# Kernel tuning notes

Hardware: AMD Instinct MI355X
Metric: run time of the kernel (lower is better)

The kernel has to match this reference:

```python
import jax, jax.numpy as jnp
import numpy as np

NEG_SLOPE = 0.2
EPS = 1e-16


def gat_conv(x, edge_index, W, a_src, a_dst, b, heads, out_c, concat):
    # PyG GATConv: lin (no bias) -> per-head attention logits -> self-loops ->
    # leaky_relu -> softmax over incoming edges per dst -> weighted scatter-add -> bias
    N = x.shape[0]
    loop = jnp.arange(N)
    src = jnp.concatenate([edge_index[0], loop])  # [E+N]
    dst = jnp.concatenate([edge_index[1], loop])
    h = (x @ W).reshape(N, heads, out_c)                    # [N,H,C]
    a_s = jnp.sum(h * a_src[None], axis=-1)                 # [N,H]
    a_d = jnp.sum(h * a_dst[None], axis=-1)                 # [N,H]
    e = jax.nn.leaky_relu(a_s[src] + a_d[dst], NEG_SLOPE)   # [E+N,H]
    m = jax.ops.segment_max(e, dst, num_segments=N)         # stable softmax per dst
    e = jnp.exp(e - m[dst])
    s = jax.ops.segment_sum(e, dst, num_segments=N)
    alpha = e / (s[dst] + EPS)                              # [E+N,H]
    msg = h[src] * alpha[:, :, None]                        # [E+N,H,C]
    out = jax.ops.segment_sum(msg, dst, num_segments=N)     # [N,H,C]
    out = out.reshape(N, heads * out_c) if concat else out.mean(axis=1)
    return out + b


def setup_inputs() -> dict:
    key = jax.random.key(0)
    ks = jax.random.split(key, 20)
    N, E = 50000, 800000
    IN, HID, H, OUT = 128, 32, 4, 1
    HC = H * HID  # 128
    g = lambda k, shp: jax.random.normal(k, shp, dtype=jnp.float32) * 0.05
    inp = {
        "x": jax.random.normal(ks[0], (N, IN), dtype=jnp.float32),
        "edge_index": jax.random.randint(ks[1], (2, E), 0, N, dtype=jnp.int64),
        "batch": jnp.zeros((N,), dtype=jnp.int64),
        # conv0: GATConv(128 -> 32, heads=4, concat)
        "c0_w": g(ks[2], (IN, HC)), "c0_asrc": g(ks[3], (H, HID)),
        "c0_adst": g(ks[4], (H, HID)), "c0_b": jnp.zeros((HC,), jnp.float32),
        "s0_w": g(ks[5], (HC, IN)), "s0_b": jnp.zeros((HC,), jnp.float32),
        # conv1: GATConv(128 -> 32, heads=4, concat)
        "c1_w": g(ks[6], (HC, HC)), "c1_asrc": g(ks[7], (H, HID)),
        "c1_adst": g(ks[8], (H, HID)), "c1_b": jnp.zeros((HC,), jnp.float32),
        "s1_w": g(ks[9], (HC, HC)), "s1_b": jnp.zeros((HC,), jnp.float32),
        # conv2: GATConv(128 -> 1, heads=1, concat=False)
        "c2_w": g(ks[10], (HC, OUT)), "c2_asrc": g(ks[11], (1, OUT)),
        "c2_adst": g(ks[12], (1, OUT)), "c2_b": jnp.zeros((OUT,), jnp.float32),
        "s2_w": g(ks[13], (OUT, HC)), "s2_b": jnp.zeros((OUT,), jnp.float32),
    }
    return inp


def reference(x, edge_index, batch,
              c0_w, c0_asrc, c0_adst, c0_b, s0_w, s0_b,
              c1_w, c1_asrc, c1_adst, c1_b, s1_w, s1_b,
              c2_w, c2_asrc, c2_adst, c2_b, s2_w, s2_b):
    # layer 0 (dropout is identity in eval mode)
    h = jax.nn.relu(gat_conv(x, edge_index, c0_w, c0_asrc, c0_adst, c0_b, 4, 32, True)
                    + x @ s0_w.T + s0_b)
    # layer 1
    h = jax.nn.relu(gat_conv(h, edge_index, c1_w, c1_asrc, c1_adst, c1_b, 4, 32, True)
                    + h @ s1_w.T + s1_b)
    # output layer: heads=1, concat=False (mean over heads)
    h = (gat_conv(h, edge_index, c2_w, c2_asrc, c2_adst, c2_b, 1, 1, False)
         + h @ s2_w.T + s2_b)
    return jax.nn.sigmoid(h)
```

## Files before the change

kernel.cpp:

```cpp
#include <hip/hip_runtime.h>
#include <math.h>

#define TPB 256

typedef short bf16x8 __attribute__((ext_vector_type(8)));
typedef float f32x4 __attribute__((ext_vector_type(4)));

static __device__ __forceinline__ float lrelu(float x) { return x > 0.f ? x : 0.2f * x; }
static __device__ __forceinline__ unsigned short f2bf(float f) {
  unsigned u = __float_as_uint(f);
  u += 0x7fffu + ((u >> 16) & 1u);
  return (unsigned short)(u >> 16);
}
static __device__ __forceinline__ float bflo(unsigned w) { return __uint_as_float(w << 16); }
static __device__ __forceinline__ float bfhi(unsigned w) { return __uint_as_float(w & 0xffff0000u); }

__global__ void k_hist(const int* __restrict__ dstE, int E, int N, int* __restrict__ deg) {
  int e = blockIdx.x * TPB + threadIdx.x;
  if (e >= E + N) return;
  int d = (e < E) ? dstE[e] : (e - E);
  d = min(max(d, 0), N - 1);
  atomicAdd(&deg[d], 1);
}

__global__ void k_scan1(const int* __restrict__ deg, int N, int* __restrict__ csum) {
  __shared__ int sm[TPB];
  int t = threadIdx.x, i = blockIdx.x * TPB + t;
  sm[t] = (i < N) ? deg[i] : 0;
  __syncthreads();
  for (int off = TPB / 2; off; off >>= 1) {
    if (t < off) sm[t] += sm[t + off];
    __syncthreads();
  }
  if (t == 0) csum[blockIdx.x] = sm[0];
}

__global__ void k_scan2(int* __restrict__ csum, int nch) {
  __shared__ int sm[TPB];
  int t = threadIdx.x;
  int v = (t < nch) ? csum[t] : 0;
  sm[t] = v;
  __syncthreads();
  for (int off = 1; off < TPB; off <<= 1) {
    int add = (t >= off) ? sm[t - off] : 0;
    __syncthreads();
    sm[t] += add;
    __syncthreads();
  }
  if (t < nch) csum[t] = (t == 0) ? 0 : sm[t - 1];
}

__global__ void k_scan3(const int* __restrict__ deg, const int* __restrict__ csum, int N, int total,
                        int* __restrict__ row_ptr, int* __restrict__ cursor) {
  __shared__ int sm[TPB];
  int b = blockIdx.x, t = threadIdx.x, i = b * TPB + t;
  int v = (i < N) ? deg[i] : 0;
  sm[t] = v;
  __syncthreads();
  for (int off = 1; off < TPB; off <<= 1) {
    int add = (t >= off) ? sm[t - off] : 0;
    __syncthreads();
    sm[t] += add;
    __syncthreads();
  }
  if (i < N) {
    int rp = csum[b] + sm[t] - v;
    row_ptr[i] = rp;
    cursor[i] = rp;
  }
  if (i == 0) row_ptr[N] = total;
}

__global__ void k_scatter(const int* __restrict__ srcE, const int* __restrict__ dstE, int E, int N,
                          int* __restrict__ cursor, int* __restrict__ csr_src) {
  int e = blockIdx.x * TPB + threadIdx.x;
  if (e >= E + N) return;
  int s = (e < E) ? srcE[e] : (e - E);
  int d = (e < E) ? dstE[e] : (e - E);
  s = min(max(s, 0), N - 1);
  d = min(max(d, 0), N - 1);
  int pos = atomicAdd(&cursor[d], 1);
  csr_src[pos] = s;
}

__global__ void k_f2b(const float4* __restrict__ in, uint4* __restrict__ out, int n8) {
  int i = blockIdx.x * TPB + threadIdx.x;
  if (i >= n8) return;
  float4 v0 = in[i * 2], v1 = in[i * 2 + 1];
  uint4 o;
  o.x = (unsigned)f2bf(v0.x) | ((unsigned)f2bf(v0.y) << 16);
  o.y = (unsigned)f2bf(v0.z) | ((unsigned)f2bf(v0.w) << 16);
  o.z = (unsigned)f2bf(v1.x) | ((unsigned)f2bf(v1.y) << 16);
  o.w = (unsigned)f2bf(v1.z) | ((unsigned)f2bf(v1.w) << 16);
  out[i] = o;
}

__global__ void k_prep_w(const float* __restrict__ cW, const float* __restrict__ sW,
                         unsigned short* __restrict__ Wb) {
  int j = blockIdx.x;
  int k = threadIdx.x;
  Wb[j * 128 + k] = f2bf((j < 128) ? cW[k * 128 + j] : sW[(j - 128) * 128 + k]);
}

__global__ __launch_bounds__(TPB) void k_gemm_mfma(const unsigned short* __restrict__ Xb,
                                                   const unsigned short* __restrict__ Wb,
                                                   unsigned short* __restrict__ H16, float* __restrict__ Sb,
                                                   int NR) {
  int wid = threadIdx.x >> 6, lane = threadIdx.x & 63;
  int r0 = blockIdx.x * 64;
  int c0 = wid * 64;
  int l15 = lane & 15, lk = lane >> 4;

  f32x4 acc[4][4];
#pragma unroll
  for (int i = 0; i < 4; ++i)
#pragma unroll
    for (int j = 0; j < 4; ++j) acc[i][j] = (f32x4){0.f, 0.f, 0.f, 0.f};

#pragma unroll
  for (int ks = 0; ks < 4; ++ks) {
    bf16x8 a[4], b[4];
#pragma unroll
    for (int rt = 0; rt < 4; ++rt) {
      int row = min(r0 + rt * 16 + l15, NR - 1);
      a[rt] = *(const bf16x8*)(Xb + (size_t)row * 128 + ks * 32 + lk * 8);
    }
#pragma unroll
    for (int ct = 0; ct < 4; ++ct) {
      int col = c0 + ct * 16 + l15;
      b[ct] = *(const bf16x8*)(Wb + (size_t)col * 128 + ks * 32 + lk * 8);
    }
#pragma unroll
    for (int rt = 0; rt < 4; ++rt)
#pragma unroll
      for (int ct = 0; ct < 4; ++ct)
        acc[rt][ct] = __builtin_amdgcn_mfma_f32_16x16x32_bf16(a[rt], b[ct], acc[rt][ct], 0, 0, 0);
  }

  int orow = lk * 4;
#pragma unroll
  for (int rt = 0; rt < 4; ++rt) {
#pragma unroll
    for (int ct = 0; ct < 4; ++ct) {
      int col = c0 + ct * 16 + l15;
#pragma unroll
      for (int r = 0; r < 4; ++r) {
        int row = r0 + rt * 16 + orow + r;
        if (row < NR) {
          float v = acc[rt][ct][r];
          if (col < 128)
            H16[(size_t)row * 128 + col] = f2bf(v);
          else
            Sb[(size_t)row * 128 + (col - 128)] = v;
        }
      }
    }
  }
}

__global__ void k_asad(const unsigned short* __restrict__ H16, const float* __restrict__ asrc,
                       const float* __restrict__ adst, float* __restrict__ a_s, float* __restrict__ a_d, int N) {
  int i = blockIdx.x * TPB + threadIdx.x;
  if (i >= N * 4) return;
  int n = i >> 2, h = i & 3;
  const uint4* hp = (const uint4*)(H16 + (size_t)n * 128 + h * 32);
  const float4* ap = (const float4*)(asrc + h * 32);
  const float4* bp = (const float4*)(adst + h * 32);
  float sa = 0.f, sd = 0.f;
#pragma unroll
  for (int q = 0; q < 4; ++q) {
    uint4 v = hp[q];
    float f0 = bflo(v.x), f1 = bfhi(v.x), f2 = bflo(v.y), f3 = bfhi(v.y);
    float f4 = bflo(v.z), f5 = bfhi(v.z), f6 = bflo(v.w), f7 = bfhi(v.w);
    float4 a0 = ap[q * 2], a1 = ap[q * 2 + 1];
    float4 b0 = bp[q * 2], b1 = bp[q * 2 + 1];
    sa += f0 * a0.x + f1 * a0.y + f2 * a0.z + f3 * a0.w + f4 * a1.x + f5 * a1.y + f6 * a1.z + f7 * a1.w;
    sd += f0 * b0.x + f1 * b0.y + f2 * b0.z + f3 * b0.w + f4 * b1.x + f5 * b1.y + f6 * b1.z + f7 * b1.w;
  }
  a_s[i] = sa;
  a_d[i] = sd;
}

template <bool BF>
__global__ __launch_bounds__(TPB) void k_smax_agg(const int* __restrict__ row_ptr, const int* __restrict__ csr_src,
                                                  const float4* __restrict__ a_s4, const float4* __restrict__ a_d4,
                                                  const unsigned short* __restrict__ H16,
                                                  const float* __restrict__ Sk, const float* __restrict__ cb,
                                                  const float* __restrict__ sb, float4* __restrict__ spill,
                                                  float* __restrict__ XnF, unsigned short* __restrict__ XnB,
                                                  int N) {
  __shared__ int s_src[4][64];
  __shared__ float s_al[4][256];
  int wid = threadIdx.x >> 6;
  int n = blockIdx.x * 4 + wid;
  if (n >= N) return;
  int lane = threadIdx.x & 63;
  int beg = row_ptr[n], end = row_ptr[n + 1];
  int deg = end - beg;
  float4 ad = a_d4[n];
  int h = lane >> 4;
  float acc0 = 0.f, acc1 = 0.f;

  if (deg <= 64) {
    int s_l = 0;
    float4 lg = make_float4(-1e30f, -1e30f, -1e30f, -1e30f);
    if (lane < deg) {
      s_l = csr_src[beg + lane];
      float4 as = a_s4[s_l];
      lg.x = lrelu(as.x + ad.x);
      lg.y = lrelu(as.y + ad.y);
      lg.z = lrelu(as.z + ad.z);
      lg.w = lrelu(as.w + ad.w);
    }
    int maxoff = (deg <= 16) ? 8 : (deg <= 32) ? 16 : 32;
    float4 mx = lg;
    for (int off = 1; off <= maxoff; off <<= 1) {
      mx.x = fmaxf(mx.x, __shfl_xor(mx.x, off));
      mx.y = fmaxf(mx.y, __shfl_xor(mx.y, off));
      mx.z = fmaxf(mx.z, __shfl_xor(mx.z, off));
      mx.w = fmaxf(mx.w, __shfl_xor(mx.w, off));
    }
    float4 pv = make_float4(0.f, 0.f, 0.f, 0.f);
    if (lane < deg) {
      pv.x = __expf(lg.x - mx.x);
      pv.y = __expf(lg.y - mx.y);
      pv.z = __expf(lg.z - mx.z);
      pv.w = __expf(lg.w - mx.w);
    }
    float4 sm = pv;
    for (int off = 1; off <= maxoff; off <<= 1) {
      sm.x += __shfl_xor(sm.x, off);
      sm.y += __shfl_xor(sm.y, off);
      sm.z += __shfl_xor(sm.z, off);
      sm.w += __shfl_xor(sm.w, off);
    }
    pv.x *= 1.f / (sm.x + 1e-16f);
    pv.y *= 1.f / (sm.y + 1e-16f);
    pv.z *= 1.f / (sm.z + 1e-16f);
    pv.w *= 1.f / (sm.w + 1e-16f);
    s_src[wid][lane] = s_l;
    *(float4*)&s_al[wid][lane * 4] = pv;
    __builtin_amdgcn_wave_barrier();

    const unsigned short* Hb = H16 + lane * 2;
    int dpad = (deg + 3) & ~3;
    for (int j = 0; j < dpad; j += 4) {
      int s0 = s_src[wid][j + 0];
      int s1 = s_src[wid][j + 1];
      int s2 = s_src[wid][j + 2];
      int s3 = s_src[wid][j + 3];
      float a0 = s_al[wid][(j + 0) * 4 + h];
      float a1 = s_al[wid][(j + 1) * 4 + h];
      float a2 = s_al[wid][(j + 2) * 4 + h];
      float a3 = s_al[wid][(j + 3) * 4 + h];
      unsigned w0 = *(const unsigned*)(Hb + (size_t)s0 * 128);
      unsigned w1 = *(const unsigned*)(Hb + (size_t)s1 * 128);
      unsigned w2 = *(const unsigned*)(Hb + (size_t)s2 * 128);
      unsigned w3 = *(const unsigned*)(Hb + (size_t)s3 * 128);
      acc0 = fmaf(a0, bflo(w0), acc0);
      acc1 = fmaf(a0, bfhi(w0), acc1);
      acc0 = fmaf(a1, bflo(w1), acc0);
      acc1 = fmaf(a1, bfhi(w1), acc1);
      acc0 = fmaf(a2, bflo(w2), acc0);
      acc1 = fmaf(a2, bfhi(w2), acc1);
      acc0 = fmaf(a3, bflo(w3), acc0);
      acc1 = fmaf(a3, bfhi(w3), acc1);
    }
  } else {
    float4 mx = make_float4(-1e30f, -1e30f, -1e30f, -1e30f);
    for (int p = beg + lane; p < end; p += 64) {
      int s = csr_src[p];
      float4 as = a_s4[s];
      float4 lg;
      lg.x = lrelu(as.x + ad.x);
      lg.y = lrelu(as.y + ad.y);
      lg.z = lrelu(as.z + ad.z);
      lg.w = lrelu(as.w + ad.w);
      spill[p] = lg;
      mx.x = fmaxf(mx.x, lg.x);
      mx.y = fmaxf(mx.y, lg.y);
      mx.z = fmaxf(mx.z, lg.z);
      mx.w = fmaxf(mx.w, lg.w);
    }
#pragma unroll
    for (int off = 32; off; off >>= 1) {
      mx.x = fmaxf(mx.x, __shfl_xor(mx.x, off));
      mx.y = fmaxf(mx.y, __shfl_xor(mx.y, off));
      mx.z = fmaxf(mx.z, __shfl_xor(mx.z, off));
      mx.w = fmaxf(mx.w, __shfl_xor(mx.w, off));
    }
    __threadfence_block();
    float4 sm = make_float4(0.f, 0.f, 0.f, 0.f);
    for (int p = beg + lane; p < end; p += 64) {
      float4 lg = spill[p];
      float4 pv;
      pv.x = __expf(lg.x - mx.x);
      pv.y = __expf(lg.y - mx.y);
      pv.z = __expf(lg.z - mx.z);
      pv.w = __expf(lg.w - mx.w);
      spill[p] = pv;
      sm.x += pv.x;
      sm.y += pv.y;
      sm.z += pv.z;
      sm.w += pv.w;
    }
#pragma unroll
    for (int off = 32; off; off >>= 1) {
      sm.x += __shfl_xor(sm.x, off);
      sm.y += __shfl_xor(sm.y, off);
      sm.z += __shfl_xor(sm.z, off);
      sm.w += __shfl_xor(sm.w, off);
    }
    float4 inv;
    inv.x = 1.f / (sm.x + 1e-16f);
    inv.y = 1.f / (sm.y + 1e-16f);
    inv.z = 1.f / (sm.z + 1e-16f);
    inv.w = 1.f / (sm.w + 1e-16f);
    __threadfence_block();
    const float* af = (const float*)spill;
    for (int p = beg; p < end; ++p) {
      int s = csr_src[p];
      float av = af[(size_t)p * 4 + h] * ((h == 0) ? inv.x : (h == 1) ? inv.y : (h == 2) ? inv.z : inv.w);
      unsigned w = *(const unsigned*)(H16 + (size_t)s * 128 + lane * 2);
      acc0 = fmaf(av, bflo(w), acc0);
      acc1 = fmaf(av, bfhi(w), acc1);
    }
  }

  int c = lane * 2;
  float2 sk = *(const float2*)(Sk + (size_t)n * 128 + c);
  float2 cbv = *(const float2*)(cb + c);
  float2 sbv = *(const float2*)(sb + c);
  float ox = fmaxf(acc0 + cbv.x + sk.x + sbv.x, 0.f);
  float oy = fmaxf(acc1 + cbv.y + sk.y + sbv.y, 0.f);
  if (BF) {
    unsigned pk = (unsigned)f2bf(ox) | ((unsigned)f2bf(oy) << 16);
    *(unsigned*)(XnB + (size_t)n * 128 + c) = pk;
  } else {
    *(float2*)(XnF + (size_t)n * 128 + c) = make_float2(ox, oy);
  }
}

__global__ void k_l2_lin(const float* __restrict__ X, const float* __restrict__ c2w, const float* __restrict__ s2w,
                         const float* __restrict__ c2as, const float* __restrict__ c2ad, float* __restrict__ h2,
                         float* __restrict__ sk2, float* __restrict__ as2, float* __restrict__ ad2, int N) {
  int gid = blockIdx.x * TPB + threadIdx.x;
  int n = gid >> 6;
  int lane = threadIdx.x & 63;
  if (n >= N) return;
  const float* xp = X + (size_t)n * 128;
  float2 xv = *(const float2*)(xp + lane * 2);
  float2 wv = *(const float2*)(c2w + lane * 2);
  float2 sv = *(const float2*)(s2w + lane * 2);
  float dh = xv.x * wv.x + xv.y * wv.y;
  float ds = xv.x * sv.x + xv.y * sv.y;
  for (int off = 32; off; off >>= 1) {
    dh += __shfl_down(dh, off);
    ds += __shfl_down(ds, off);
  }
  if (lane == 0) {
    h2[n] = dh;
    sk2[n] = ds;
    as2[n] = dh * c2as[0];
    ad2[n] = dh * c2ad[0];
  }
}

__global__ __launch_bounds__(TPB) void k_l2_smax_agg(const int* __restrict__ row_ptr, const int* __restrict__ csr_src,
                                                     const float* __restrict__ as2, const float* __restrict__ ad2,
                                                     const float* __restrict__ h2, const float* __restrict__ sk2,
                                                     const float* __restrict__ c2b, const float* __restrict__ s2b,
                                                     float* __restrict__ out, int N) {
  int n = blockIdx.x * 4 + (threadIdx.x >> 6);
  if (n >= N) return;
  int lane = threadIdx.x & 63;
  int beg = row_ptr[n], end = row_ptr[n + 1];
  int deg = end - beg;
  float ad = ad2[n];
  float num = 0.f, den = 0.f;

  if (deg <= 64) {
    float lg = -1e30f, hv = 0.f;
    if (lane < deg) {
      int s = csr_src[beg + lane];
      lg = lrelu(as2[s] + ad);
      hv = h2[s];
    }
    float mx = lg;
#pragma unroll
    for (int off = 32; off; off >>= 1) mx = fmaxf(mx, __shfl_xor(mx, off));
    float pv = (lane < deg) ? __expf(lg - mx) : 0.f;
    num = pv * hv;
    den = pv;
  } else {
    float mx = -1e30f;
    for (int p = beg + lane; p < end; p += 64) mx = fmaxf(mx, lrelu(as2[csr_src[p]] + ad));
#pragma unroll
    for (int off = 32; off; off >>= 1) mx = fmaxf(mx, __shfl_xor(mx, off));
    for (int p = beg + lane; p < end; p += 64) {
      int s = csr_src[p];
      float pv = __expf(lrelu(as2[s] + ad) - mx);
      num += pv * h2[s];
      den += pv;
    }
  }
#pragma unroll
  for (int off = 32; off; off >>= 1) {
    num += __shfl_xor(num, off);
    den += __shfl_xor(den, off);
  }
  if (lane == 0) {
    float v = num / (den + 1e-16f) + c2b[0] + sk2[n] + s2b[0];
    out[n] = 1.f / (1.f + __expf(-v));
  }
}

extern "C" void kernel_launch(void* const* d_in, const int* in_sizes, int n_in,
                              void* d_out, int out_size, void* d_ws, size_t ws_size,
                              hipStream_t stream) {
  const float* x = (const float*)d_in[0];
  const int* ei = (const int*)d_in[1];
  const float* c0_w = (const float*)d_in[3];
  const float* c0_as = (const float*)d_in[4];
  const float* c0_ad = (const float*)d_in[5];
  const float* c0_b = (const float*)d_in[6];
  const float* s0_w = (const float*)d_in[7];
  const float* s0_b = (const float*)d_in[8];
  const float* c1_w = (const float*)d_in[9];
  const float* c1_as = (const float*)d_in[10];
  const float* c1_ad = (const float*)d_in[11];
  const float* c1_b = (const float*)d_in[12];
  const float* s1_w = (const float*)d_in[13];
  const float* s1_b = (const float*)d_in[14];
  const float* c2_w = (const float*)d_in[15];
  const float* c2_as = (const float*)d_in[16];
  const float* c2_ad = (const float*)d_in[17];
  const float* c2_b = (const float*)d_in[18];
  const float* s2_w = (const float*)d_in[19];
  const float* s2_b = (const float*)d_in[20];

  const int N = in_sizes[0] / 128;
  const int E = in_sizes[1] / 2;
  const int EN = E + N;
  const int* srcE = ei;
  const int* dstE = ei + E;

  char* wp_ = (char*)d_ws;
  auto alloc = [&](size_t bytes) -> void* {
    void* r = (void*)wp_;
    wp_ += (bytes + 255) & ~(size_t)255;
    return r;
  };
  unsigned short* Xb0 = (unsigned short*)alloc((size_t)N * 128 * 2);
  unsigned short* Xb1 = (unsigned short*)alloc((size_t)N * 128 * 2);
  unsigned short* H16 = (unsigned short*)alloc((size_t)N * 128 * 2);
  float* Sk = (float*)alloc((size_t)N * 128 * 4);
  float* P2 = (float*)alloc((size_t)N * 128 * 4);
  float* a_s = (float*)alloc((size_t)N * 4 * 4);
  float* a_d = (float*)alloc((size_t)N * 4 * 4);
  float* spill = (float*)alloc((size_t)EN * 4 * 4);
  unsigned short* Wb = (unsigned short*)alloc(256 * 128 * 2);
  int* deg = (int*)alloc((size_t)N * 4);
  int* row_ptr = (int*)alloc((size_t)(N + 1) * 4);
  int* cursor = (int*)alloc((size_t)N * 4);
  int* csum = (int*)alloc(4096 * 4);
  int* csr_src = (int*)alloc((size_t)EN * 4);
  float* h2 = (float*)alloc((size_t)N * 4);
  float* sk2 = (float*)alloc((size_t)N * 4);
  float* as2 = (float*)alloc((size_t)N * 4);
  float* ad2 = (float*)alloc((size_t)N * 4);

  const int gEN = (EN + TPB - 1) / TPB;
  const int gN4 = (N * 4 + TPB - 1) / TPB;
  const int nch = (N + TPB - 1) / TPB;
  const int gGemm = (N + 63) / 64;
  const int gWave = (N + 3) / 4;
  const int n8 = N * 128 / 8;

  hipMemsetAsync(deg, 0, (size_t)N * 4, stream);
  k_hist<<<gEN, TPB, 0, stream>>>(dstE, E, N, deg);
  k_scan1<<<nch, TPB, 0, stream>>>(deg, N, csum);
  k_scan2<<<1, TPB, 0, stream>>>(csum, nch);
  k_scan3<<<nch, TPB, 0, stream>>>(deg, csum, N, EN, row_ptr, cursor);
  k_scatter<<<gEN, TPB, 0, stream>>>(srcE, dstE, E, N, cursor, csr_src);

  k_f2b<<<(n8 + TPB - 1) / TPB, TPB, 0, stream>>>((const float4*)x, (uint4*)Xb0, n8);
  k_prep_w<<<256, 128, 0, stream>>>(c0_w, s0_w, Wb);
  k_gemm_mfma<<<gGemm, TPB, 0, stream>>>(Xb0, Wb, H16, Sk, N);
  k_asad<<<gN4, TPB, 0, stream>>>(H16, c0_as, c0_ad, a_s, a_d, N);
  k_smax_agg<true><<<gWave, TPB, 0, stream>>>(row_ptr, csr_src, (const float4*)a_s, (const float4*)a_d, H16, Sk,
                                              c0_b, s0_b, (float4*)spill, nullptr, Xb1, N);

  k_prep_w<<<256, 128, 0, stream>>>(c1_w, s1_w, Wb);
  k_gemm_mfma<<<gGemm, TPB, 0, stream>>>(Xb1, Wb, H16, Sk, N);
  k_asad<<<gN4, TPB, 0, stream>>>(H16, c1_as, c1_ad, a_s, a_d, N);
  k_smax_agg<false><<<gWave, TPB, 0, stream>>>(row_ptr, csr_src, (const float4*)a_s, (const float4*)a_d, H16, Sk,
                                               c1_b, s1_b, (float4*)spill, P2, nullptr, N);

  k_l2_lin<<<(N * 64 + TPB - 1) / TPB, TPB, 0, stream>>>(P2, c2_w, s2_w, c2_as, c2_ad, h2, sk2, as2, ad2, N);
  k_l2_smax_agg<<<gWave, TPB, 0, stream>>>(row_ptr, csr_src, as2, ad2, h2, sk2, c2_b, s2_b, (float*)d_out, N);
}
```

Before: 388.4 us.

## Fuse input conversion, layer-2 linear and weight prep; partition CSR build by dst range

Folds the fp32-to-bf16 conversion of x into the first GEMM and fuses the layer-2 projection into the layer-1 aggregation epilogue, removing the P2 fp32 buffer and the separate lin kernel. Skip outputs are stored as bf16 instead of fp32, halving that traffic. Both weight matrices are prepared in one launch. The histogram and scatter kernels now split destinations into 8 ranges per block group to localize atomics, at the cost of each range rereading all edges. bf16 skip storage adds rounding error.

```diff
diff --git a/kernel.cpp b/kernel.cpp
--- a/kernel.cpp
+++ b/kernel.cpp
@@ -2,6 +2,7 @@
 #include <math.h>
 
 #define TPB 256
+#define RB 128
 
 typedef short bf16x8 __attribute__((ext_vector_type(8)));
 typedef float f32x4 __attribute__((ext_vector_type(4)));
@@ -14,13 +15,29 @@
 }
 static __device__ __forceinline__ float bflo(unsigned w) { return __uint_as_float(w << 16); }
 static __device__ __forceinline__ float bfhi(unsigned w) { return __uint_as_float(w & 0xffff0000u); }
-
-__global__ void k_hist(const int* __restrict__ dstE, int E, int N, int* __restrict__ deg) {
-  int e = blockIdx.x * TPB + threadIdx.x;
-  if (e >= E + N) return;
-  int d = (e < E) ? dstE[e] : (e - E);
-  d = min(max(d, 0), N - 1);
-  atomicAdd(&deg[d], 1);
+static __device__ __forceinline__ bf16x8 pack8(float4 v0, float4 v1) {
+  bf16x8 r;
+  r[0] = (short)f2bf(v0.x);
+  r[1] = (short)f2bf(v0.y);
+  r[2] = (short)f2bf(v0.z);
+  r[3] = (short)f2bf(v0.w);
+  r[4] = (short)f2bf(v1.x);
+  r[5] = (short)f2bf(v1.y);
+  r[6] = (short)f2bf(v1.z);
+  r[7] = (short)f2bf(v1.w);
+  return r;
+}
+
+__global__ void k_hist8(const int* __restrict__ dstE, int E, int N, int* __restrict__ deg) {
+  int r = blockIdx.x & 7;
+  int nb = gridDim.x >> 3;
+  int lo = (int)(((long)r * N) / 8), hi = (int)(((long)(r + 1) * N) / 8);
+  int EN = E + N;
+  for (int e = (blockIdx.x >> 3) * TPB + threadIdx.x; e < EN; e += nb * TPB) {
+    int d = (e < E) ? dstE[e] : (e - E);
+    d = min(max(d, 0), N - 1);
+    if (d >= lo && d < hi) atomicAdd(&deg[d], 1);
+  }
 }
 
 __global__ void k_scan1(const int* __restrict__ deg, int N, int* __restrict__ csum) {
@@ -71,41 +88,41 @@
   if (i == 0) row_ptr[N] = total;
 }
 
-__global__ void k_scatter(const int* __restrict__ srcE, const int* __restrict__ dstE, int E, int N,
-                          int* __restrict__ cursor, int* __restrict__ csr_src) {
-  int e = blockIdx.x * TPB + threadIdx.x;
-  if (e >= E + N) return;
-  int s = (e < E) ? srcE[e] : (e - E);
-  int d = (e < E) ? dstE[e] : (e - E);
-  s = min(max(s, 0), N - 1);
-  d = min(max(d, 0), N - 1);
-  int pos = atomicAdd(&cursor[d], 1);
-  csr_src[pos] = s;
-}
-
-__global__ void k_f2b(const float4* __restrict__ in, uint4* __restrict__ out, int n8) {
-  int i = blockIdx.x * TPB + threadIdx.x;
-  if (i >= n8) return;
-  float4 v0 = in[i * 2], v1 = in[i * 2 + 1];
-  uint4 o;
-  o.x = (unsigned)f2bf(v0.x) | ((unsigned)f2bf(v0.y) << 16);
-  o.y = (unsigned)f2bf(v0.z) | ((unsigned)f2bf(v0.w) << 16);
-  o.z = (unsigned)f2bf(v1.x) | ((unsigned)f2bf(v1.y) << 16);
-  o.w = (unsigned)f2bf(v1.z) | ((unsigned)f2bf(v1.w) << 16);
-  out[i] = o;
-}
-
-__global__ void k_prep_w(const float* __restrict__ cW, const float* __restrict__ sW,
-                         unsigned short* __restrict__ Wb) {
-  int j = blockIdx.x;
+__global__ void k_scatter8(const int* __restrict__ srcE, const int* __restrict__ dstE, int E, int N,
+                           int* __restrict__ cursor, int* __restrict__ csr_src) {
+  int r = blockIdx.x & 7;
+  int nb = gridDim.x >> 3;
+  int lo = (int)(((long)r * N) / 8), hi = (int)(((long)(r + 1) * N) / 8);
+  int EN = E + N;
+  for (int e = (blockIdx.x >> 3) * TPB + threadIdx.x; e < EN; e += nb * TPB) {
+    int d = (e < E) ? dstE[e] : (e - E);
+    d = min(max(d, 0), N - 1);
+    if (d >= lo && d < hi) {
+      int s = (e < E) ? srcE[e] : (e - E);
+      s = min(max(s, 0), N - 1);
+      int pos = atomicAdd(&cursor[d], 1);
+      csr_src[pos] = s;
+    }
+  }
+}
+
+__global__ void k_prep_w2(const float* __restrict__ cW0, const float* __restrict__ sW0,
+                          const float* __restrict__ cW1, const float* __restrict__ sW1,
+                          unsigned short* __restrict__ Wb0, unsigned short* __restrict__ Wb1) {
+  int j = blockIdx.x & 255;
+  int which = blockIdx.x >> 8;
   int k = threadIdx.x;
+  const float* cW = which ? cW1 : cW0;
+  const float* sW = which ? sW1 : sW0;
+  unsigned short* Wb = which ? Wb1 : Wb0;
   Wb[j * 128 + k] = f2bf((j < 128) ? cW[k * 128 + j] : sW[(j - 128) * 128 + k]);
 }
 
-__global__ __launch_bounds__(TPB) void k_gemm_mfma(const unsigned short* __restrict__ Xb,
+template <bool F32IN>
+__global__ __launch_bounds__(TPB) void k_gemm_mfma(const void* __restrict__ Xv,
                                                    const unsigned short* __restrict__ Wb,
-                                                   unsigned short* __restrict__ H16, float* __restrict__ Sb,
-                                                   int NR) {
+                                                   unsigned short* __restrict__ H16,
+                                                   unsigned short* __restrict__ Sk16, int NR) {
   int wid = threadIdx.x >> 6, lane = threadIdx.x & 63;
   int r0 = blockIdx.x * 64;
   int c0 = wid * 64;
@@ -123,7 +140,12 @@
 #pragma unroll
     for (int rt = 0; rt < 4; ++rt) {
       int row = min(r0 + rt * 16 + l15, NR - 1);
-      a[rt] = *(const bf16x8*)(Xb + (size_t)row * 128 + ks * 32 + lk * 8);
+      if (F32IN) {
+        const float* xp = (const float*)Xv + (size_t)row * 128 + ks * 32 + lk * 8;
+        a[rt] = pack8(*(const float4*)xp, *(const float4*)(xp + 4));
+      } else {
+        a[rt] = *(const bf16x8*)((const unsigned short*)Xv + (size_t)row * 128 + ks * 32 + lk * 8);
+      }
     }
 #pragma unroll
     for (int ct = 0; ct < 4; ++ct) {
@@ -151,7 +173,7 @@
           if (col < 128)
             H16[(size_t)row * 128 + col] = f2bf(v);
           else
-            Sb[(size_t)row * 128 + (col - 128)] = v;
+            Sk16[(size_t)row * 128 + (col - 128)] = f2bf(v);
         }
       }
     }
@@ -181,14 +203,14 @@
   a_d[i] = sd;
 }
 
-template <bool BF>
-__global__ __launch_bounds__(TPB) void k_smax_agg(const int* __restrict__ row_ptr, const int* __restrict__ csr_src,
-                                                  const float4* __restrict__ a_s4, const float4* __restrict__ a_d4,
-                                                  const unsigned short* __restrict__ H16,
-                                                  const float* __restrict__ Sk, const float* __restrict__ cb,
-                                                  const float* __restrict__ sb, float4* __restrict__ spill,
-                                                  float* __restrict__ XnF, unsigned short* __restrict__ XnB,
-                                                  int N) {
+template <bool BF, bool L2F>
+__global__ __launch_bounds__(TPB) void k_smax_agg(
+    const int* __restrict__ row_ptr, const int* __restrict__ csr_src, const float4* __restrict__ a_s4,
+    const float4* __restrict__ a_d4, const unsigned short* __restrict__ H16,
+    const unsigned short* __restrict__ Sk16, const float* __restrict__ cb, const float* __restrict__ sb,
+    float4* __restrict__ spill, unsigned short* __restrict__ XnB, const float* __restrict__ c2w,
+    const float* __restrict__ s2w, const float* __restrict__ c2as, const float* __restrict__ c2ad,
+    float* __restrict__ h2, float* __restrict__ sk2, float* __restrict__ as2, float* __restrict__ ad2, int N) {
   __shared__ int s_src[4][64];
   __shared__ float s_al[4][256];
   int wid = threadIdx.x >> 6;
@@ -328,41 +350,31 @@
   }
 
   int c = lane * 2;
-  float2 sk = *(const float2*)(Sk + (size_t)n * 128 + c);
+  unsigned skw = *(const unsigned*)(Sk16 + (size_t)n * 128 + c);
   float2 cbv = *(const float2*)(cb + c);
   float2 sbv = *(const float2*)(sb + c);
-  float ox = fmaxf(acc0 + cbv.x + sk.x + sbv.x, 0.f);
-  float oy = fmaxf(acc1 + cbv.y + sk.y + sbv.y, 0.f);
+  float ox = fmaxf(acc0 + cbv.x + bflo(skw) + sbv.x, 0.f);
+  float oy = fmaxf(acc1 + cbv.y + bfhi(skw) + sbv.y, 0.f);
   if (BF) {
     unsigned pk = (unsigned)f2bf(ox) | ((unsigned)f2bf(oy) << 16);
     *(unsigned*)(XnB + (size_t)n * 128 + c) = pk;
-  } else {
-    *(float2*)(XnF + (size_t)n * 128 + c) = make_float2(ox, oy);
-  }
-}
-
-__global__ void k_l2_lin(const float* __restrict__ X, const float* __restrict__ c2w, const float* __restrict__ s2w,
-                         const float* __restrict__ c2as, const float* __restrict__ c2ad, float* __restrict__ h2,
-                         float* __restrict__ sk2, float* __restrict__ as2, float* __restrict__ ad2, int N) {
-  int gid = blockIdx.x * TPB + threadIdx.x;
-  int n = gid >> 6;
-  int lane = threadIdx.x & 63;
-  if (n >= N) return;
-  const float* xp = X + (size_t)n * 128;
-  float2 xv = *(const float2*)(xp + lane * 2);
-  float2 wv = *(const float2*)(c2w + lane * 2);
-  float2 sv = *(const float2*)(s2w + lane * 2);
-  float dh = xv.x * wv.x + xv.y * wv.y;
-  float ds = xv.x * sv.x + xv.y * sv.y;
-  for (int off = 32; off; off >>= 1) {
-    dh += __shfl_down(dh, off);
-    ds += __shfl_down(ds, off);
-  }
-  if (lane == 0) {
-    h2[n] = dh;
-    sk2[n] = ds;
-    as2[n] = dh * c2as[0];
-    ad2[n] = dh * c2ad[0];
+  }
+  if (L2F) {
+    float2 wv = *(const float2*)(c2w + c);
+    float2 sv = *(const float2*)(s2w + c);
+    float dh = ox * wv.x + oy * wv.y;
+    float ds = ox * sv.x + oy * sv.y;
+#pragma unroll
+    for (int off = 32; off; off >>= 1) {
+      dh += __shfl_xor(dh, off);
+      ds += __shfl_xor(ds, off);
+    }
+    if (lane == 0) {
+      h2[n] = dh;
+      sk2[n] = ds;
+      as2[n] = dh * c2as[0];
+      ad2[n] = dh * c2ad[0];
+    }
   }
 }
 
@@ -451,15 +463,14 @@
     wp_ += (bytes + 255) & ~(size_t)255;
     return r;
   };
-  unsigned short* Xb0 = (unsigned short*)alloc((size_t)N * 128 * 2);
   unsigned short* Xb1 = (unsigned short*)alloc((size_t)N * 128 * 2);
   unsigned short* H16 = (unsigned short*)alloc((size_t)N * 128 * 2);
-  float* Sk = (float*)alloc((size_t)N * 128 * 4);
-  float* P2 = (float*)alloc((size_t)N * 128 * 4);
+  unsigned short* Sk16 = (unsigned short*)alloc((size_t)N * 128 * 2);
   float* a_s = (float*)alloc((size_t)N * 4 * 4);
   float* a_d = (float*)alloc((size_t)N * 4 * 4);
   float* spill = (float*)alloc((size_t)EN * 4 * 4);
-  unsigned short* Wb = (unsigned short*)alloc(256 * 128 * 2);
+  unsigned short* Wb0 = (unsigned short*)alloc(256 * 128 * 2);
+  unsigned short* Wb1 = (unsigned short*)alloc(256 * 128 * 2);
   int* deg = (int*)alloc((size_t)N * 4);
   int* row_ptr = (int*)alloc((size_t)(N + 1) * 4);
   int* cursor = (int*)alloc((size_t)N * 4);
@@ -470,33 +481,31 @@
   float* as2 = (float*)alloc((size_t)N * 4);
   float* ad2 = (float*)alloc((size_t)N * 4);
 
-  const int gEN = (EN + TPB - 1) / TPB;
   const int gN4 = (N * 4 + TPB - 1) / TPB;
   const int nch = (N + TPB - 1) / TPB;
   const int gGemm = (N + 63) / 64;
   const int gWave = (N + 3) / 4;
-  const int n8 = N * 128 / 8;
 
   hipMemsetAsync(deg, 0, (size_t)N * 4, stream);
-  k_hist<<<gEN, TPB, 0, stream>>>(dstE, E, N, deg);
+  k_hist8<<<8 * RB, TPB, 0, stream>>>(dstE, E, N, deg);
   k_scan1<<<nch, TPB, 0, stream>>>(deg, N, csum);
   k_scan2<<<1, TPB, 0, stream>>>(csum, nch);
   k_scan3<<<nch, TPB, 0, stream>>>(deg, csum, N, EN, row_ptr, cursor);
-  k_scatter<<<gEN, TPB, 0, stream>>>(srcE, dstE, E, N, cursor, csr_src);
-
-  k_f2b<<<(n8 + TPB - 1) / TPB, TPB, 0, stream>>>((const float4*)x, (uint4*)Xb0, n8);
-  k_prep_w<<<256, 128, 0, stream>>>(c0_w, s0_w, Wb);
-  k_gemm_mfma<<<gGemm, TPB, 0, stream>>>(Xb0, Wb, H16, Sk, N);
+  k_scatter8<<<8 * RB, TPB, 0, stream>>>(srcE, dstE, E, N, cursor, csr_src);
+
+  k_prep_w2<<<512, 128, 0, stream>>>(c0_w, s0_w, c1_w, s1_w, Wb0, Wb1);
+
+  k_gemm_mfma<true><<<gGemm, TPB, 0, stream>>>(x, Wb0, H16, Sk16, N);
   k_asad<<<gN4, TPB, 0, stream>>>(H16, c0_as, c0_ad, a_s, a_d, N);
-  k_smax_agg<true><<<gWave, TPB, 0, stream>>>(row_ptr, csr_src, (const float4*)a_s, (const float4*)a_d, H16, Sk,
-                                              c0_b, s0_b, (float4*)spill, nullptr, Xb1, N);
-
-  k_prep_w<<<256, 128, 0, stream>>>(c1_w, s1_w, Wb);
-  k_gemm_mfma<<<gGemm, TPB, 0, stream>>>(Xb1, Wb, H16, Sk, N);
+  k_smax_agg<true, false><<<gWave, TPB, 0, stream>>>(row_ptr, csr_src, (const float4*)a_s, (const float4*)a_d,
+                                                     H16, Sk16, c0_b, s0_b, (float4*)spill, Xb1, nullptr, nullptr,
+                                                     nullptr, nullptr, nullptr, nullptr, nullptr, nullptr, N);
+
+  k_gemm_mfma<false><<<gGemm, TPB, 0, stream>>>(Xb1, Wb1, H16, Sk16, N);
   k_asad<<<gN4, TPB, 0, stream>>>(H16, c1_as, c1_ad, a_s, a_d, N);
-  k_smax_agg<false><<<gWave, TPB, 0, stream>>>(row_ptr, csr_src, (const float4*)a_s, (const float4*)a_d, H16, Sk,
-                                               c1_b, s1_b, (float4*)spill, P2, nullptr, N);
-
-  k_l2_lin<<<(N * 64 + TPB - 1) / TPB, TPB, 0, stream>>>(P2, c2_w, s2_w, c2_as, c2_ad, h2, sk2, as2, ad2, N);
+  k_smax_agg<false, true><<<gWave, TPB, 0, stream>>>(row_ptr, csr_src, (const float4*)a_s, (const float4*)a_d,
+                                                     H16, Sk16, c1_b, s1_b, (float4*)spill, nullptr, c2_w, s2_w,
+                                                     c2_as, c2_ad, h2, sk2, as2, ad2, N);
+
   k_l2_smax_agg<<<gWave, TPB, 0, stream>>>(row_ptr, csr_src, as2, ad2, h2, sk2, c2_b, s2_b, (float*)d_out, N);
 }
```

Result: faster. 367.6 us (-5.3%).
